# Kernel tuning notes

Measured on AMD Instinct MI355X. Metric: run time of the kernel, lower is better.

The kernel has to match this reference:

```python
import jax, jax.numpy as jnp
import numpy as np

N, T, C, H, W = 16, 8, 256, 14, 14
IC = 64          # inter_channels
SCALE = 32       # nearest-upsample factor (scale_s); scale_t = 1


def setup_inputs() -> dict:
    key = jax.random.key(0)
    kx, kq1, kq2, kv1, kl, ki = jax.random.split(key, 6)
    cin = C + 1
    x = jax.random.normal(kx, (N, T, C, H, W), dtype=jnp.float32)
    lam = jax.random.uniform(kl, (), dtype=jnp.float32)
    index = jax.random.randint(ki, (N,), 0, N)
    # nn.Linear default init: U(-1/sqrt(fan_in), 1/sqrt(fan_in))
    bound = 1.0 / np.sqrt(cin)
    Wq = jax.random.uniform(kq1, (IC, cin), minval=-bound, maxval=bound, dtype=jnp.float32)
    bq = jax.random.uniform(kq2, (IC,), minval=-bound, maxval=bound, dtype=jnp.float32)
    Wv = jax.random.uniform(kv1, (1, cin), minval=-bound, maxval=bound, dtype=jnp.float32)
    Wv = Wv.at[0, C].set(4.0)   # value.weight.data[0, in_channel] = 4
    bv = jnp.zeros((1,), dtype=jnp.float32)  # value.bias.data[:] = 0
    return {"x": x, "lam": lam, "index": index, "Wq": Wq, "bq": bq, "Wv": Wv, "bv": bv}


def reference(x, lam, index, Wq, bq, Wv, bv):
    n, t, c, h, w = x.shape
    ic = Wq.shape[0]
    nt, hw = n * t, h * w
    x_lam = x.reshape(nt, c, h, w)
    x_lam_ = x[index].reshape(nt, c, h, w)           # batch-shuffled partner
    lam_block = jnp.broadcast_to(lam - 0.5, (nt, 1, h, w)).astype(x.dtype)
    x_lam = jnp.concatenate([x_lam, lam_block], axis=1)     # [nt, c+1, h, w]
    x_lam_ = jnp.concatenate([x_lam_, -lam_block], axis=1)
    # linear over channel dim (equivalent to the transpose(1,3)/Linear/transpose dance)
    q = jnp.einsum('nchw,dc->ndhw', x_lam, Wq) + bq[None, :, None, None]
    k = jnp.einsum('nchw,dc->ndhw', x_lam_, Wq) + bq[None, :, None, None]
    v = jnp.einsum('nchw,dc->ndhw', x_lam_, Wv) + bv[None, :, None, None]
    q_x = q.reshape(nt, ic, hw).transpose(0, 2, 1)   # [nt, hw, ic]
    k_x = k.reshape(nt, ic, hw)                      # [nt, ic, hw]
    v_ = v.reshape(nt, 1, hw).transpose(0, 2, 1)     # [nt, hw, 1]
    scores = jnp.einsum('nqd,ndk->nqk', q_x, k_x) / jnp.sqrt(jnp.float32(ic))
    attn = jax.nn.softmax(scores, axis=-1)           # [nt, hw, hw]
    mask_lam_ = jnp.matmul(attn.astype(jnp.float32), v_.astype(jnp.float32))
    mask_lam_ = mask_lam_.reshape(nt, 1, h, w)       # scale_t == 1 so expand is a no-op
    # F.interpolate(mode='nearest', scale_factor=SCALE)
    mask_lam_ = jnp.repeat(jnp.repeat(mask_lam_, SCALE, axis=2), SCALE, axis=3)
    mask_lam_ = jax.nn.sigmoid(mask_lam_)
    mask = jnp.concatenate([1.0 - mask_lam_, mask_lam_], axis=1)  # [nt, 2, h*S, w*S]
    v_out = v_.reshape(n, t, h, w)                    # (n, t*scale_t, h, w)
    return mask, v_out
```

## Files before the change

### kernel.cpp

```cpp
#include <hip/hip_runtime.h>
#include <hip/hip_bf16.h>
#include <stdint.h>

#define HWsz 196
#define NTs  128
#define MASK_ELEMS 51380224
#define VOUT_OFF   MASK_ELEMS
#define MASK_CHUNKS 6422528

#define WLAM_OFF 8192
#define BQ_OFF   8256
#define WV_OFF   8320
#define LAM_OFF  8577
#define BV_OFF   8578
#define EQ_OFF_F 3221504
#define EK_OFF_F 4024704
#define V_OFF    4827904
#define SIG_OFF  4852992

typedef __attribute__((ext_vector_type(8))) short short8;
typedef __attribute__((ext_vector_type(4))) float f32x4;

__device__ __forceinline__ bool is_bf16_mode(const void* wv) {
  return ((const uint16_t*)wv)[256] == (uint16_t)0x4080;
}

__device__ __forceinline__ float ldf(const void* p, int i, bool bf) {
  if (bf) {
    uint32_t u = (uint32_t)((const uint16_t*)p)[i] << 16;
    return __builtin_bit_cast(float, u);
  }
  return ((const float*)p)[i];
}

__device__ __forceinline__ uint16_t f2bf(float f) {
  __hip_bfloat16 h = __float2bfloat16(f);
  return __builtin_bit_cast(uint16_t, h);
}

__device__ __forceinline__ float bf2f(uint16_t u) {
  uint32_t v = (uint32_t)u << 16;
  return __builtin_bit_cast(float, v);
}

__global__ __launch_bounds__(256) void k0_prep(const void* Wq, const void* bq,
                                               const void* Wv, const void* lam,
                                               const void* bv, float* ws) {
  int idx = blockIdx.x * 256 + threadIdx.x;
  bool bf = is_bf16_mode(Wv);
  if (idx < 16384) {
    int d = idx >> 8, c = idx & 255;
    ((uint16_t*)ws)[idx] = f2bf(ldf(Wq, d * 257 + c, bf));
  } else if (idx < 16448) {
    int d = idx - 16384;
    ws[WLAM_OFF + d] = ldf(Wq, d * 257 + 256, bf);
  } else if (idx < 16512) {
    ws[BQ_OFF + idx - 16448] = ldf(bq, idx - 16448, bf);
  } else if (idx < 16769) {
    ws[WV_OFF + idx - 16512] = ldf(Wv, idx - 16512, bf);
  } else if (idx == 16769) {
    ws[LAM_OFF] = ldf(lam, 0, bf) - 0.5f;
  } else if (idx == 16770) {
    ws[BV_OFF] = ldf(bv, 0, bf);
  }
}

__global__ __launch_bounds__(256) void k1_qk(const void* xraw, const int* index,
                                             const void* Wvraw, float* ws, void* dout) {
  __shared__ __align__(16) uint16_t Abuf[64 * 200];
  __shared__ __align__(16) uint16_t Bbuf[208 * 64];
  int b = blockIdx.x;
  int isK = (b >= NTs) ? 1 : 0;
  int s = isK ? b - NTs : b;
  int t = s & 7;
  int src = isK ? index[s >> 3] * 8 + t : s;
  bool bf = is_bf16_mode(Wvraw);
  int tid = threadIdx.x;
  int lane = tid & 63, w = tid >> 6;
  int ln = lane & 15, quad = lane >> 4;

  const uint16_t* wqb = (const uint16_t*)ws;
  size_t xbase = (size_t)src * 256 * 196;

  f32x4 acc[13];
#pragma unroll
  for (int mt = 0; mt < 13; mt++) acc[mt] = (f32x4){0.f, 0.f, 0.f, 0.f};
  float vacc = 0.f;

#pragma unroll 1
  for (int chunk = 0; chunk < 4; chunk++) {
    __syncthreads();
    if (bf) {
      for (int i2 = tid; i2 < 3136; i2 += 256) {
        int c = i2 / 49, jj = i2 - c * 49;
        uint2 val = *(const uint2*)((const uint16_t*)xraw + xbase +
                                    (size_t)(chunk * 64 + c) * 196 + jj * 4);
        *(uint2*)(Abuf + c * 200 + jj * 4) = val;
      }
    } else {
      for (int i2 = tid; i2 < 3136; i2 += 256) {
        int c = i2 / 49, jj = i2 - c * 49;
        float4 v4 = *(const float4*)((const float*)xraw + xbase +
                                     (size_t)(chunk * 64 + c) * 196 + jj * 4);
        uint2 pk;
        pk.x = (uint32_t)f2bf(v4.x) | ((uint32_t)f2bf(v4.y) << 16);
        pk.y = (uint32_t)f2bf(v4.z) | ((uint32_t)f2bf(v4.w) << 16);
        *(uint2*)(Abuf + c * 200 + jj * 4) = pk;
      }
    }
    __syncthreads();
    for (int i = tid; i < 6272; i += 256) {
      int c2 = i / 196, j = i - c2 * 196;
      uint32_t lo = Abuf[(2 * c2) * 200 + j];
      uint32_t hi = Abuf[(2 * c2 + 1) * 200 + j];
      int g  = c2 >> 2;
      int gp = g ^ (j & 7);
      ((uint32_t*)Bbuf)[j * 32 + gp * 4 + (c2 & 3)] = lo | (hi << 16);
    }
    __syncthreads();
#pragma unroll
    for (int kc2 = 0; kc2 < 2; kc2++) {
      short8 bfrag = *(const short8*)(wqb + (size_t)(w * 16 + ln) * 256 +
                                      chunk * 64 + kc2 * 32 + quad * 8);
      int gp = (kc2 * 4 + quad) ^ (ln & 7);
#pragma unroll
      for (int mt = 0; mt < 13; mt++) {
        int j = mt * 16 + ln;
        short8 afrag = *(const short8*)(Bbuf + j * 64 + ((kc2 * 4 + quad) ^ (j & 7)) * 8);
        (void)gp;
        acc[mt] = __builtin_amdgcn_mfma_f32_16x16x32_bf16(afrag, bfrag, acc[mt], 0, 0, 0);
      }
    }
    if (isK && tid < HWsz) {
      const float* wvp = ws + WV_OFF + chunk * 64;
#pragma unroll 4
      for (int c = 0; c < 64; c++)
        vacc = fmaf(bf2f(Abuf[c * 200 + tid]), wvp[c], vacc);
    }
  }

  float lamv = ws[LAM_OFF];
  float lamch = isK ? -lamv : lamv;
  int d = w * 16 + ln;
  float addend = ws[WLAM_OFF + d] * lamch + ws[BQ_OFF + d];
  uint16_t* E = (uint16_t*)(ws + (isK ? EK_OFF_F : EQ_OFF_F));
#pragma unroll
  for (int mt = 0; mt < 13; mt++) {
#pragma unroll
    for (int r = 0; r < 4; r++) {
      int j = mt * 16 + quad * 4 + r;
      if (j < HWsz) E[((size_t)s * HWsz + j) * 64 + d] = f2bf(acc[mt][r] + addend);
    }
  }

  if (isK && tid < HWsz) {
    float vvv = vacc + ws[WV_OFF + 256] * lamch + ws[BV_OFF];
    ws[V_OFF + s * HWsz + tid] = vvv;
    bool outbf = bf;
    if (outbf) ((uint16_t*)dout)[VOUT_OFF + s * HWsz + tid] = f2bf(vvv);
    else       ((float*)dout)[VOUT_OFF + s * HWsz + tid] = vvv;
  }
}

__global__ __launch_bounds__(256) void k2_attn(float* ws) {
  int s = blockIdx.x >> 2, blk = blockIdx.x & 3;
  int lane = threadIdx.x & 63, w = threadIdx.x >> 6;
  int mt = blk * 4 + w;
  if (mt >= 13) return;
  int ln = lane & 15, quad = lane >> 4;
  const uint16_t* Eq = (const uint16_t*)(ws + EQ_OFF_F);
  const uint16_t* Ek = (const uint16_t*)(ws + EK_OFF_F);

  const uint16_t* qrow = Eq + ((size_t)s * 196 + mt * 16 + ln) * 64 + quad * 8;
  short8 aq0 = *(const short8*)(qrow);
  short8 aq1 = *(const short8*)(qrow + 32);

  float vcol[13];
  f32x4 acc[13];
#pragma unroll
  for (int nt = 0; nt < 13; nt++) {
    int col = nt * 16 + ln;
    vcol[nt] = (col < 196) ? ws[V_OFF + s * 196 + col] : 0.f;
    const uint16_t* krow = Ek + ((size_t)s * 196 + col) * 64 + quad * 8;
    short8 b0 = *(const short8*)(krow);
    short8 b1 = *(const short8*)(krow + 32);
    f32x4 a = (f32x4){0.f, 0.f, 0.f, 0.f};
    a = __builtin_amdgcn_mfma_f32_16x16x32_bf16(aq0, b0, a, 0, 0, 0);
    a = __builtin_amdgcn_mfma_f32_16x16x32_bf16(aq1, b1, a, 0, 0, 0);
    acc[nt] = a;
  }

  float mx[4] = {-1e30f, -1e30f, -1e30f, -1e30f};
#pragma unroll
  for (int nt = 0; nt < 13; nt++) {
    bool valid = (nt * 16 + ln) < 196;
#pragma unroll
    for (int r = 0; r < 4; r++) {
      float sv = valid ? acc[nt][r] * 0.125f : -1e30f;
      acc[nt][r] = sv;
      mx[r] = fmaxf(mx[r], sv);
    }
  }
#pragma unroll
  for (int m = 1; m < 16; m <<= 1)
#pragma unroll
    for (int r = 0; r < 4; r++) mx[r] = fmaxf(mx[r], __shfl_xor(mx[r], m));

  float l[4] = {0.f, 0.f, 0.f, 0.f}, av[4] = {0.f, 0.f, 0.f, 0.f};
#pragma unroll
  for (int nt = 0; nt < 13; nt++)
#pragma unroll
    for (int r = 0; r < 4; r++) {
      float p = __expf(acc[nt][r] - mx[r]);
      l[r] += p;
      av[r] += p * vcol[nt];
    }
#pragma unroll
  for (int m = 1; m < 16; m <<= 1)
#pragma unroll
    for (int r = 0; r < 4; r++) {
      l[r] += __shfl_xor(l[r], m);
      av[r] += __shfl_xor(av[r], m);
    }

  if (ln == 0) {
#pragma unroll
    for (int r = 0; r < 4; r++) {
      int j = mt * 16 + quad * 4 + r;
      if (j < 196) {
        float mval = av[r] / l[r];
        ws[SIG_OFF + s * 196 + j] = 1.f / (1.f + __expf(-mval));
      }
    }
  }
}

__global__ __launch_bounds__(256) void k3_mask(const float* ws, void* dout, const void* Wvraw) {
  bool bf = is_bf16_mode(Wvraw);
  int stride = gridDim.x * 256;
  for (int idx = blockIdx.x * 256 + threadIdx.x; idx < MASK_CHUNKS; idx += stride) {
    int c8  = idx % 56;
    int row = idx / 56;
    int y   = row % 448;
    int tmp = row / 448;
    float m = ws[SIG_OFF + (tmp >> 1) * HWsz + (y >> 5) * 14 + (c8 >> 2)];
    float val = (tmp & 1) ? m : 1.0f - m;
    if (bf) {
      uint32_t ub = (uint32_t)f2bf(val);
      uint32_t pk = ub | (ub << 16);
      uint4 qv; qv.x = pk; qv.y = pk; qv.z = pk; qv.w = pk;
      ((uint4*)dout)[idx] = qv;
    } else {
      float4 f = make_float4(val, val, val, val);
      ((float4*)dout)[(size_t)idx * 2]     = f;
      ((float4*)dout)[(size_t)idx * 2 + 1] = f;
    }
  }
}

extern "C" void kernel_launch(void* const* d_in, const int* in_sizes, int n_in,
                              void* d_out, int out_size, void* d_ws, size_t ws_size,
                              hipStream_t stream) {
  const void* x   = d_in[0];
  const void* lam = d_in[1];
  const int* idx  = (const int*)d_in[2];
  const void* Wq  = d_in[3];
  const void* bq  = d_in[4];
  const void* Wv  = d_in[5];
  const void* bv  = d_in[6];
  float* ws = (float*)d_ws;

  k0_prep<<<66, 256, 0, stream>>>(Wq, bq, Wv, lam, bv, ws);
  k1_qk<<<256, 256, 0, stream>>>(x, idx, Wv, ws, d_out);
  k2_attn<<<512, 256, 0, stream>>>(ws);
  k3_mask<<<6272, 256, 0, stream>>>(ws, d_out, Wv);
}
```

Baseline: 274.5 us.

## Fuse attention with mask upsample, drop prep kernel, split QK projection by columns

Removes the weight-prep kernel: k1 now reads Wq, bq, Wv, lam and bv directly from the raw inputs and converts to bf16 inline. k1 is split into two column halves (112 and 84 spatial positions), doubling the grid to 512 blocks for better occupancy and smaller LDS. The separate mask kernel is fused into the attention kernel, which keeps the sigmoid values in shared memory and writes the upsampled mask directly, so a launch and a workspace round trip go away. The cost is redundant Wq loads and conversions per block, and a mask write done by only 512 blocks, which may use bandwidth less well.

```diff
diff --git a/kernel.cpp b/kernel.cpp
--- a/kernel.cpp
+++ b/kernel.cpp
@@ -6,17 +6,10 @@
 #define NTs  128
 #define MASK_ELEMS 51380224
 #define VOUT_OFF   MASK_ELEMS
-#define MASK_CHUNKS 6422528
-
-#define WLAM_OFF 8192
-#define BQ_OFF   8256
-#define WV_OFF   8320
-#define LAM_OFF  8577
-#define BV_OFF   8578
+
 #define EQ_OFF_F 3221504
 #define EK_OFF_F 4024704
 #define V_OFF    4827904
-#define SIG_OFF  4852992
 
 typedef __attribute__((ext_vector_type(8))) short short8;
 typedef __attribute__((ext_vector_type(4))) float f32x4;
@@ -43,217 +36,222 @@
   return __builtin_bit_cast(float, v);
 }
 
-__global__ __launch_bounds__(256) void k0_prep(const void* Wq, const void* bq,
-                                               const void* Wv, const void* lam,
-                                               const void* bv, float* ws) {
-  int idx = blockIdx.x * 256 + threadIdx.x;
-  bool bf = is_bf16_mode(Wv);
-  if (idx < 16384) {
-    int d = idx >> 8, c = idx & 255;
-    ((uint16_t*)ws)[idx] = f2bf(ldf(Wq, d * 257 + c, bf));
-  } else if (idx < 16448) {
-    int d = idx - 16384;
-    ws[WLAM_OFF + d] = ldf(Wq, d * 257 + 256, bf);
-  } else if (idx < 16512) {
-    ws[BQ_OFF + idx - 16448] = ldf(bq, idx - 16448, bf);
-  } else if (idx < 16769) {
-    ws[WV_OFF + idx - 16512] = ldf(Wv, idx - 16512, bf);
-  } else if (idx == 16769) {
-    ws[LAM_OFF] = ldf(lam, 0, bf) - 0.5f;
-  } else if (idx == 16770) {
-    ws[BV_OFF] = ldf(bv, 0, bf);
-  }
-}
-
-__global__ __launch_bounds__(256) void k1_qk(const void* xraw, const int* index,
-                                             const void* Wvraw, float* ws, void* dout) {
-  __shared__ __align__(16) uint16_t Abuf[64 * 200];
-  __shared__ __align__(16) uint16_t Bbuf[208 * 64];
-  int b = blockIdx.x;
-  int isK = (b >= NTs) ? 1 : 0;
-  int s = isK ? b - NTs : b;
+#define AST 116
+
+template<int NMT, int NCOLS, int J0>
+__device__ __forceinline__ void k1_body(uint16_t* Abuf, uint16_t* Bbuf,
+    const void* xraw, const int* index, const void* Wqraw, const void* bqraw,
+    const void* Wvraw, const void* bvraw, const void* lamraw,
+    float* ws, void* dout, int b) {
+  int s = b & 127, isK = (b >> 7) & 1;
   int t = s & 7;
   int src = isK ? index[s >> 3] * 8 + t : s;
   bool bf = is_bf16_mode(Wvraw);
   int tid = threadIdx.x;
   int lane = tid & 63, w = tid >> 6;
   int ln = lane & 15, quad = lane >> 4;
-
-  const uint16_t* wqb = (const uint16_t*)ws;
+  int d = w * 16 + ln;
   size_t xbase = (size_t)src * 256 * 196;
 
-  f32x4 acc[13];
-#pragma unroll
-  for (int mt = 0; mt < 13; mt++) acc[mt] = (f32x4){0.f, 0.f, 0.f, 0.f};
+  f32x4 acc[NMT];
+#pragma unroll
+  for (int mt = 0; mt < NMT; mt++) acc[mt] = (f32x4){0.f, 0.f, 0.f, 0.f};
   float vacc = 0.f;
+  int cS1 = tid >> 2, jjS1 = tid & 3;
+  int c2S = tid >> 3, jtS = tid & 7;
 
 #pragma unroll 1
   for (int chunk = 0; chunk < 4; chunk++) {
+    short8 bw0, bw1;
+    {
+      int cb = d * 257 + chunk * 64 + quad * 8;
+#pragma unroll
+      for (int e = 0; e < 8; e++) {
+        bw0[e] = (short)f2bf(ldf(Wqraw, cb + e, bf));
+        bw1[e] = (short)f2bf(ldf(Wqraw, cb + 32 + e, bf));
+      }
+    }
     __syncthreads();
     if (bf) {
-      for (int i2 = tid; i2 < 3136; i2 += 256) {
-        int c = i2 / 49, jj = i2 - c * 49;
-        uint2 val = *(const uint2*)((const uint16_t*)xraw + xbase +
-                                    (size_t)(chunk * 64 + c) * 196 + jj * 4);
-        *(uint2*)(Abuf + c * 200 + jj * 4) = val;
-      }
+      const uint16_t* xp = (const uint16_t*)xraw + xbase +
+                           (size_t)(chunk * 64 + cS1) * 196 + J0;
+      for (int jj = jjS1; jj * 4 < NCOLS; jj += 4)
+        *(uint2*)(Abuf + cS1 * AST + jj * 4) = *(const uint2*)(xp + jj * 4);
     } else {
-      for (int i2 = tid; i2 < 3136; i2 += 256) {
-        int c = i2 / 49, jj = i2 - c * 49;
-        float4 v4 = *(const float4*)((const float*)xraw + xbase +
-                                     (size_t)(chunk * 64 + c) * 196 + jj * 4);
+      const float* xp = (const float*)xraw + xbase +
+                        (size_t)(chunk * 64 + cS1) * 196 + J0;
+      for (int jj = jjS1; jj * 4 < NCOLS; jj += 4) {
+        float4 v4 = *(const float4*)(xp + jj * 4);
         uint2 pk;
         pk.x = (uint32_t)f2bf(v4.x) | ((uint32_t)f2bf(v4.y) << 16);
         pk.y = (uint32_t)f2bf(v4.z) | ((uint32_t)f2bf(v4.w) << 16);
-        *(uint2*)(Abuf + c * 200 + jj * 4) = pk;
+        *(uint2*)(Abuf + cS1 * AST + jj * 4) = pk;
       }
     }
     __syncthreads();
-    for (int i = tid; i < 6272; i += 256) {
-      int c2 = i / 196, j = i - c2 * 196;
-      uint32_t lo = Abuf[(2 * c2) * 200 + j];
-      uint32_t hi = Abuf[(2 * c2 + 1) * 200 + j];
-      int g  = c2 >> 2;
-      int gp = g ^ (j & 7);
-      ((uint32_t*)Bbuf)[j * 32 + gp * 4 + (c2 & 3)] = lo | (hi << 16);
+    for (int j = jtS; j < NCOLS; j += 8) {
+      uint32_t lo = Abuf[(2 * c2S) * AST + j];
+      uint32_t hi = Abuf[(2 * c2S + 1) * AST + j];
+      int gp = (c2S >> 2) ^ (j & 7);
+      ((uint32_t*)Bbuf)[j * 32 + gp * 4 + (c2S & 3)] = lo | (hi << 16);
     }
     __syncthreads();
 #pragma unroll
     for (int kc2 = 0; kc2 < 2; kc2++) {
-      short8 bfrag = *(const short8*)(wqb + (size_t)(w * 16 + ln) * 256 +
-                                      chunk * 64 + kc2 * 32 + quad * 8);
-      int gp = (kc2 * 4 + quad) ^ (ln & 7);
-#pragma unroll
-      for (int mt = 0; mt < 13; mt++) {
+      short8 bfrag = kc2 ? bw1 : bw0;
+#pragma unroll
+      for (int mt = 0; mt < NMT; mt++) {
         int j = mt * 16 + ln;
-        short8 afrag = *(const short8*)(Bbuf + j * 64 + ((kc2 * 4 + quad) ^ (j & 7)) * 8);
-        (void)gp;
+        short8 afrag = *(const short8*)(Bbuf + j * 64 +
+                                        (((kc2 * 4 + quad) ^ (j & 7)) << 3));
         acc[mt] = __builtin_amdgcn_mfma_f32_16x16x32_bf16(afrag, bfrag, acc[mt], 0, 0, 0);
       }
     }
-    if (isK && tid < HWsz) {
-      const float* wvp = ws + WV_OFF + chunk * 64;
-#pragma unroll 4
+    if (isK && tid < NCOLS) {
+#pragma unroll 8
       for (int c = 0; c < 64; c++)
-        vacc = fmaf(bf2f(Abuf[c * 200 + tid]), wvp[c], vacc);
-    }
-  }
-
-  float lamv = ws[LAM_OFF];
+        vacc = fmaf(bf2f(Abuf[c * AST + tid]), ldf(Wvraw, chunk * 64 + c, bf), vacc);
+    }
+  }
+
+  float lamv = ldf(lamraw, 0, bf) - 0.5f;
   float lamch = isK ? -lamv : lamv;
-  int d = w * 16 + ln;
-  float addend = ws[WLAM_OFF + d] * lamch + ws[BQ_OFF + d];
+  float addend = ldf(Wqraw, d * 257 + 256, bf) * lamch + ldf(bqraw, d, bf);
   uint16_t* E = (uint16_t*)(ws + (isK ? EK_OFF_F : EQ_OFF_F));
 #pragma unroll
-  for (int mt = 0; mt < 13; mt++) {
+  for (int mt = 0; mt < NMT; mt++) {
 #pragma unroll
     for (int r = 0; r < 4; r++) {
-      int j = mt * 16 + quad * 4 + r;
+      int j = J0 + mt * 16 + quad * 4 + r;
       if (j < HWsz) E[((size_t)s * HWsz + j) * 64 + d] = f2bf(acc[mt][r] + addend);
     }
   }
 
-  if (isK && tid < HWsz) {
-    float vvv = vacc + ws[WV_OFF + 256] * lamch + ws[BV_OFF];
-    ws[V_OFF + s * HWsz + tid] = vvv;
-    bool outbf = bf;
-    if (outbf) ((uint16_t*)dout)[VOUT_OFF + s * HWsz + tid] = f2bf(vvv);
-    else       ((float*)dout)[VOUT_OFF + s * HWsz + tid] = vvv;
-  }
-}
-
-__global__ __launch_bounds__(256) void k2_attn(float* ws) {
+  if (isK && tid < NCOLS) {
+    int j = J0 + tid;
+    float vvv = vacc + ldf(Wvraw, 256, bf) * lamch + ldf(bvraw, 0, bf);
+    ws[V_OFF + s * HWsz + j] = vvv;
+    if (bf) ((uint16_t*)dout)[VOUT_OFF + s * HWsz + j] = f2bf(vvv);
+    else    ((float*)dout)[VOUT_OFF + s * HWsz + j] = vvv;
+  }
+}
+
+__global__ __launch_bounds__(256) void k1_qk(const void* xraw, const int* index,
+    const void* Wqraw, const void* bqraw, const void* Wvraw, const void* bvraw,
+    const void* lamraw, float* ws, void* dout) {
+  __shared__ __align__(16) uint16_t Abuf[64 * AST];
+  __shared__ __align__(16) uint16_t Bbuf[112 * 64];
+  int b = blockIdx.x;
+  if (b < 256)
+    k1_body<7, 112, 0>(Abuf, Bbuf, xraw, index, Wqraw, bqraw, Wvraw, bvraw, lamraw, ws, dout, b);
+  else
+    k1_body<6, 84, 112>(Abuf, Bbuf, xraw, index, Wqraw, bqraw, Wvraw, bvraw, lamraw, ws, dout, b & 255);
+}
+
+__global__ __launch_bounds__(256) void k2_attn_mask(float* ws, void* dout, const void* Wvraw) {
+  __shared__ float sig[64];
+  bool bf = is_bf16_mode(Wvraw);
   int s = blockIdx.x >> 2, blk = blockIdx.x & 3;
-  int lane = threadIdx.x & 63, w = threadIdx.x >> 6;
+  int tid = threadIdx.x;
+  int lane = tid & 63, w = tid >> 6;
   int mt = blk * 4 + w;
-  if (mt >= 13) return;
   int ln = lane & 15, quad = lane >> 4;
-  const uint16_t* Eq = (const uint16_t*)(ws + EQ_OFF_F);
-  const uint16_t* Ek = (const uint16_t*)(ws + EK_OFF_F);
-
-  const uint16_t* qrow = Eq + ((size_t)s * 196 + mt * 16 + ln) * 64 + quad * 8;
-  short8 aq0 = *(const short8*)(qrow);
-  short8 aq1 = *(const short8*)(qrow + 32);
-
-  float vcol[13];
-  f32x4 acc[13];
-#pragma unroll
-  for (int nt = 0; nt < 13; nt++) {
-    int col = nt * 16 + ln;
-    vcol[nt] = (col < 196) ? ws[V_OFF + s * 196 + col] : 0.f;
-    const uint16_t* krow = Ek + ((size_t)s * 196 + col) * 64 + quad * 8;
-    short8 b0 = *(const short8*)(krow);
-    short8 b1 = *(const short8*)(krow + 32);
-    f32x4 a = (f32x4){0.f, 0.f, 0.f, 0.f};
-    a = __builtin_amdgcn_mfma_f32_16x16x32_bf16(aq0, b0, a, 0, 0, 0);
-    a = __builtin_amdgcn_mfma_f32_16x16x32_bf16(aq1, b1, a, 0, 0, 0);
-    acc[nt] = a;
-  }
-
-  float mx[4] = {-1e30f, -1e30f, -1e30f, -1e30f};
-#pragma unroll
-  for (int nt = 0; nt < 13; nt++) {
-    bool valid = (nt * 16 + ln) < 196;
-#pragma unroll
-    for (int r = 0; r < 4; r++) {
-      float sv = valid ? acc[nt][r] * 0.125f : -1e30f;
-      acc[nt][r] = sv;
-      mx[r] = fmaxf(mx[r], sv);
-    }
-  }
-#pragma unroll
-  for (int m = 1; m < 16; m <<= 1)
-#pragma unroll
-    for (int r = 0; r < 4; r++) mx[r] = fmaxf(mx[r], __shfl_xor(mx[r], m));
-
-  float l[4] = {0.f, 0.f, 0.f, 0.f}, av[4] = {0.f, 0.f, 0.f, 0.f};
-#pragma unroll
-  for (int nt = 0; nt < 13; nt++)
-#pragma unroll
-    for (int r = 0; r < 4; r++) {
-      float p = __expf(acc[nt][r] - mx[r]);
-      l[r] += p;
-      av[r] += p * vcol[nt];
-    }
-#pragma unroll
-  for (int m = 1; m < 16; m <<= 1)
-#pragma unroll
-    for (int r = 0; r < 4; r++) {
-      l[r] += __shfl_xor(l[r], m);
-      av[r] += __shfl_xor(av[r], m);
-    }
-
-  if (ln == 0) {
-#pragma unroll
-    for (int r = 0; r < 4; r++) {
-      int j = mt * 16 + quad * 4 + r;
-      if (j < 196) {
-        float mval = av[r] / l[r];
-        ws[SIG_OFF + s * 196 + j] = 1.f / (1.f + __expf(-mval));
-      }
-    }
-  }
-}
-
-__global__ __launch_bounds__(256) void k3_mask(const float* ws, void* dout, const void* Wvraw) {
-  bool bf = is_bf16_mode(Wvraw);
-  int stride = gridDim.x * 256;
-  for (int idx = blockIdx.x * 256 + threadIdx.x; idx < MASK_CHUNKS; idx += stride) {
-    int c8  = idx % 56;
-    int row = idx / 56;
-    int y   = row % 448;
-    int tmp = row / 448;
-    float m = ws[SIG_OFF + (tmp >> 1) * HWsz + (y >> 5) * 14 + (c8 >> 2)];
-    float val = (tmp & 1) ? m : 1.0f - m;
-    if (bf) {
-      uint32_t ub = (uint32_t)f2bf(val);
-      uint32_t pk = ub | (ub << 16);
-      uint4 qv; qv.x = pk; qv.y = pk; qv.z = pk; qv.w = pk;
-      ((uint4*)dout)[idx] = qv;
-    } else {
-      float4 f = make_float4(val, val, val, val);
-      ((float4*)dout)[(size_t)idx * 2]     = f;
-      ((float4*)dout)[(size_t)idx * 2 + 1] = f;
+
+  if (mt < 13) {
+    const uint16_t* Eq = (const uint16_t*)(ws + EQ_OFF_F);
+    const uint16_t* Ek = (const uint16_t*)(ws + EK_OFF_F);
+    const uint16_t* qrow = Eq + ((size_t)s * 196 + mt * 16 + ln) * 64 + quad * 8;
+    short8 aq0 = *(const short8*)(qrow);
+    short8 aq1 = *(const short8*)(qrow + 32);
+
+    float vcol[13];
+    f32x4 acc[13];
+#pragma unroll
+    for (int nt = 0; nt < 13; nt++) {
+      int col = nt * 16 + ln;
+      vcol[nt] = (col < 196) ? ws[V_OFF + s * 196 + col] : 0.f;
+      const uint16_t* krow = Ek + ((size_t)s * 196 + col) * 64 + quad * 8;
+      short8 b0 = *(const short8*)(krow);
+      short8 b1 = *(const short8*)(krow + 32);
+      f32x4 a = (f32x4){0.f, 0.f, 0.f, 0.f};
+      a = __builtin_amdgcn_mfma_f32_16x16x32_bf16(aq0, b0, a, 0, 0, 0);
+      a = __builtin_amdgcn_mfma_f32_16x16x32_bf16(aq1, b1, a, 0, 0, 0);
+      acc[nt] = a;
+    }
+
+    float mx[4] = {-1e30f, -1e30f, -1e30f, -1e30f};
+#pragma unroll
+    for (int nt = 0; nt < 13; nt++) {
+      bool valid = (nt * 16 + ln) < 196;
+#pragma unroll
+      for (int r = 0; r < 4; r++) {
+        float sv = valid ? acc[nt][r] * 0.125f : -1e30f;
+        acc[nt][r] = sv;
+        mx[r] = fmaxf(mx[r], sv);
+      }
+    }
+#pragma unroll
+    for (int m = 1; m < 16; m <<= 1)
+#pragma unroll
+      for (int r = 0; r < 4; r++) mx[r] = fmaxf(mx[r], __shfl_xor(mx[r], m));
+
+    float l[4] = {0.f, 0.f, 0.f, 0.f}, av[4] = {0.f, 0.f, 0.f, 0.f};
+#pragma unroll
+    for (int nt = 0; nt < 13; nt++)
+#pragma unroll
+      for (int r = 0; r < 4; r++) {
+        float p = __expf(acc[nt][r] - mx[r]);
+        l[r] += p;
+        av[r] += p * vcol[nt];
+      }
+#pragma unroll
+    for (int m = 1; m < 16; m <<= 1)
+#pragma unroll
+      for (int r = 0; r < 4; r++) {
+        l[r] += __shfl_xor(l[r], m);
+        av[r] += __shfl_xor(av[r], m);
+      }
+
+    if (ln == 0) {
+#pragma unroll
+      for (int r = 0; r < 4; r++) {
+        int j = mt * 16 + quad * 4 + r;
+        if (j < 196) {
+          float mval = av[r] / l[r];
+          sig[j & 63] = 1.f / (1.f + __expf(-mval));
+        }
+      }
+    }
+  }
+  __syncthreads();
+
+  int j0 = blk * 64;
+  int nrows = (blk == 3) ? 4 : 64;
+  int base2 = s * 2;
+  if (!bf) {
+    float4* o4 = (float4*)dout;
+    int total = nrows << 9;
+    for (int i = tid; i < total; i += 256) {
+      int x4 = i & 7, dy = (i >> 3) & 31, ch = (i >> 8) & 1, jl = i >> 9;
+      int j = j0 + jl;
+      int yhw = j / 14, xhw = j - yhw * 14;
+      float v = sig[jl];
+      if (!ch) v = 1.f - v;
+      size_t off4 = (size_t)(base2 + ch) * 50176 + (yhw * 32 + dy) * 112 + (xhw << 3) + x4;
+      o4[off4] = make_float4(v, v, v, v);
+    }
+  } else {
+    uint4* o = (uint4*)dout;
+    int total = nrows << 8;
+    for (int i = tid; i < total; i += 256) {
+      int x4 = i & 3, dy = (i >> 2) & 31, ch = (i >> 7) & 1, jl = i >> 8;
+      int j = j0 + jl;
+      int yhw = j / 14, xhw = j - yhw * 14;
+      float v = sig[jl];
+      if (!ch) v = 1.f - v;
+      uint32_t ub = (uint32_t)f2bf(v), pk = ub | (ub << 16);
+      size_t off = (size_t)(base2 + ch) * 25088 + (yhw * 32 + dy) * 56 + (xhw << 2) + x4;
+      o[off] = (uint4){pk, pk, pk, pk};
     }
   }
 }
@@ -270,8 +268,6 @@
   const void* bv  = d_in[6];
   float* ws = (float*)d_ws;
 
-  k0_prep<<<66, 256, 0, stream>>>(Wq, bq, Wv, lam, bv, ws);
-  k1_qk<<<256, 256, 0, stream>>>(x, idx, Wv, ws, d_out);
-  k2_attn<<<512, 256, 0, stream>>>(ws);
-  k3_mask<<<6272, 256, 0, stream>>>(ws, d_out, Wv);
-}
+  k1_qk<<<512, 256, 0, stream>>>(x, idx, Wq, bq, Wv, bv, lam, ws, d_out);
+  k2_attn_mask<<<512, 256, 0, stream>>>(ws, d_out, Wv);
+}
```

After: 265.9 us. 3.2% less time.
